# Kernel optimization log

Measured on AMD Instinct MI355X. Metric: run time of the kernel, lower is better.

The kernel has to match this reference:

```python
import jax, jax.numpy as jnp
import numpy as np

# FNO 2D spectral conv: rfft2 -> keep 2 corner mode blocks -> complex einsum -> scatter -> irfft2
B, H, W, CIN, COUT = 8, 256, 256, 32, 32
M1, M2 = 16, 16
SCALE = 1.0 / (CIN * COUT)  # matches self.scale = 1/(in_channels*out_channels)


def setup_inputs() -> dict:
    key = jax.random.key(0)
    k1, k2, k3 = jax.random.split(key, 3)
    x = jax.random.normal(k1, (B, H, W, CIN), dtype=jnp.float32)  # channels_last input
    wshape = (2, CIN, COUT, M1, M2)  # (2**(ndims-1), in_c, out_c, m1, m2)
    w_real = (jax.random.uniform(k2, wshape, dtype=jnp.float32) * 2.0 - 1.0) * SCALE
    w_imag = (jax.random.uniform(k3, wshape, dtype=jnp.float32) * 2.0 - 1.0) * SCALE
    return {"x": x, "w_real": w_real, "w_imag": w_imag}


def reference(x, w_real, w_imag):
    w = jax.lax.complex(w_real, w_imag)  # complex64 spectral weights
    # channels_last -> channels_first: [B,H,W,C] -> [B,C,H,W]
    xc = jnp.transpose(x, (0, 3, 1, 2))
    x_ft = jnp.fft.rfft2(xc)  # [B, C, H, W//2+1] complex64
    # Two corner blocks along dim H (low and high freqs), low freqs along rfft dim.
    blocks = jnp.stack(
        [x_ft[:, :, :M1, :M2], x_ft[:, :, H - M1:, :M2]], axis=0
    )  # [2, B, Cin, M1, M2]
    # einsum 'wbi...,wio...->w...bo' (reordered here to wbohk; scatter layout equivalent)
    ob = jnp.einsum('wbihk,wiohk->wbohk', blocks, w)  # [2, B, Cout, M1, M2]
    out_ft = jnp.zeros((B, COUT, H, W // 2 + 1), dtype=ob.dtype)
    out_ft = out_ft.at[:, :, :M1, :M2].set(ob[0])
    out_ft = out_ft.at[:, :, H - M1:, :M2].set(ob[1])
    out = jnp.fft.irfft2(out_ft, s=(H, W))  # [B, Cout, H, W] float32
    # back to channels_last; activation is None (identity)
    return jnp.transpose(out, (0, 2, 3, 1))
```

## Files before the change

kernel.cpp:

```cpp
#include <hip/hip_runtime.h>
#include <math.h>


#define INV_HW (1.0f / 65536.0f)

__global__ void k_tw(float* __restrict__ Eo, float* __restrict__ Ei,
                     float* __restrict__ U, float* __restrict__ E4) {
  int t = blockIdx.x * blockDim.x + threadIdx.x;
  const float step = 6.28318530717958647692f / 256.0f;
  if (t < 512) {
    int j = t & 3, kwq = (t >> 2) & 3, w1 = (t >> 4) & 15, ws = t >> 8;
    int kw = 4 * kwq + j, w = ws * 64 + 4 * w1;
    int m = (kw * w) & 255;
    float s, c; sincosf(step * (float)m, &s, &c);
    int base = ((ws * 16 + w1) * 4 + kwq) * 8 + 2 * j;
    Eo[base] = c; Eo[base + 1] = -s;
  } else if (t < 576) {
    int i = t - 512;
    int j = i & 3, w0 = (i >> 2) & 3, kwq = i >> 4;
    int kw = 4 * kwq + j;
    int m = (kw * w0) & 255;
    float s, c; sincosf(step * (float)m, &s, &c);
    int base = (kwq * 4 + w0) * 8 + 2 * j;
    Ei[base] = c; Ei[base + 1] = -s;
  } else if (t < 832) {
    int n = t - 576;
    float s, c; sincosf(step * (float)n, &s, &c);
    ((float2*)U)[n] = make_float2(c, s);
  } else if (t < 1856) {
    int i = t - 832;
    int w = i >> 3, q = i & 7;
    int me = (2 * q * w) & 255, mo = ((2 * q + 1) * w) & 255;
    float se, ce, so, co;
    sincosf(step * (float)me, &se, &ce);
    sincosf(step * (float)mo, &so, &co);
    float sc_e = (q == 0) ? INV_HW : 2.0f * INV_HW;
    float sc_o = 2.0f * INV_HW;
    ((float4*)E4)[i] = make_float4(sc_e * ce, sc_e * se, sc_o * co, sc_o * so);
  }
}

__global__ __launch_bounds__(256) void k_wdft(const float* __restrict__ x,
                                              const float* __restrict__ Eo,
                                              const float* __restrict__ Ei,
                                              float* __restrict__ T) {
  __shared__ __align__(16) float sx[8192];
  __shared__ __align__(16) float sEo[1024];
  __shared__ __align__(16) float sEi[128];
  int bh = blockIdx.x, t = threadIdx.x;
  const float4* src = (const float4*)(x + (size_t)bh * 8192);
  float4* dx = (float4*)sx;
#pragma unroll
  for (int i = 0; i < 8; ++i) dx[t + 256 * i] = src[t + 256 * i];
  ((float4*)sEo)[t] = ((const float4*)Eo)[t];
  if (t < 32) ((float4*)sEi)[t] = ((const float4*)Ei)[t];
  __syncthreads();
  int kwq = t >> 6, ws = (t >> 5) & 1, c = t & 31;
  float ar[4][4], ai[4][4];
#pragma unroll
  for (int a = 0; a < 4; ++a)
#pragma unroll
    for (int b = 0; b < 4; ++b) { ar[a][b] = 0.f; ai[a][b] = 0.f; }
  const float* xc = sx + c;
#pragma unroll 4
  for (int w1 = 0; w1 < 16; ++w1) {
    int wb = ws * 64 + 4 * w1;
    float xa0 = xc[(wb + 0) * 32], xa1 = xc[(wb + 1) * 32];
    float xa2 = xc[(wb + 2) * 32], xa3 = xc[(wb + 3) * 32];
    float xb0 = xc[(wb + 128) * 32], xb1 = xc[(wb + 129) * 32];
    float xb2 = xc[(wb + 130) * 32], xb3 = xc[(wb + 131) * 32];
    const float4* ep = (const float4*)(sEo + ((ws * 16 + w1) * 4 + kwq) * 8);
    float4 e01 = ep[0], e23 = ep[1];
    float ye, yo;
    ye = xa0 + xb0; yo = xa0 - xb0;
    ar[0][0] += ye * e01.x; ai[0][0] += ye * e01.y;
    ar[0][1] += yo * e01.z; ai[0][1] += yo * e01.w;
    ar[0][2] += ye * e23.x; ai[0][2] += ye * e23.y;
    ar[0][3] += yo * e23.z; ai[0][3] += yo * e23.w;
    ye = xa1 + xb1; yo = xa1 - xb1;
    ar[1][0] += ye * e01.x; ai[1][0] += ye * e01.y;
    ar[1][1] += yo * e01.z; ai[1][1] += yo * e01.w;
    ar[1][2] += ye * e23.x; ai[1][2] += ye * e23.y;
    ar[1][3] += yo * e23.z; ai[1][3] += yo * e23.w;
    ye = xa2 + xb2; yo = xa2 - xb2;
    ar[2][0] += ye * e01.x; ai[2][0] += ye * e01.y;
    ar[2][1] += yo * e01.z; ai[2][1] += yo * e01.w;
    ar[2][2] += ye * e23.x; ai[2][2] += ye * e23.y;
    ar[2][3] += yo * e23.z; ai[2][3] += yo * e23.w;
    ye = xa3 + xb3; yo = xa3 - xb3;
    ar[3][0] += ye * e01.x; ai[3][0] += ye * e01.y;
    ar[3][1] += yo * e01.z; ai[3][1] += yo * e01.w;
    ar[3][2] += ye * e23.x; ai[3][2] += ye * e23.y;
    ar[3][3] += yo * e23.z; ai[3][3] += yo * e23.w;
  }
  const float4* eip = (const float4*)(sEi + kwq * 32);
  float Tr[4] = {0, 0, 0, 0}, Ti[4] = {0, 0, 0, 0};
#pragma unroll
  for (int w0 = 0; w0 < 4; ++w0) {
    float4 g01 = eip[2 * w0], g23 = eip[2 * w0 + 1];
    Tr[0] += ar[w0][0] * g01.x - ai[w0][0] * g01.y;
    Ti[0] += ar[w0][0] * g01.y + ai[w0][0] * g01.x;
    Tr[1] += ar[w0][1] * g01.z - ai[w0][1] * g01.w;
    Ti[1] += ar[w0][1] * g01.w + ai[w0][1] * g01.z;
    Tr[2] += ar[w0][2] * g23.x - ai[w0][2] * g23.y;
    Ti[2] += ar[w0][2] * g23.y + ai[w0][2] * g23.x;
    Tr[3] += ar[w0][3] * g23.z - ai[w0][3] * g23.w;
    Ti[3] += ar[w0][3] * g23.w + ai[w0][3] * g23.z;
  }
#pragma unroll
  for (int j = 0; j < 4; ++j) {
    Tr[j] += __shfl_xor(Tr[j], 32);
    Ti[j] += __shfl_xor(Ti[j], 32);
  }
  if (ws == 0) {
    float* tp = T + (size_t)bh * 1024 + c * 32 + kwq * 8;
    *(float4*)tp = make_float4(Tr[0], Ti[0], Tr[1], Ti[1]);
    *(float4*)(tp + 4) = make_float4(Tr[2], Ti[2], Tr[3], Ti[3]);
  }
}

__global__ __launch_bounds__(256) void k_hdft(const float* __restrict__ T,
                                              const float* __restrict__ U,
                                              float* __restrict__ Xp) {
  __shared__ __align__(16) float sT[2048];
  __shared__ float2 sU[256];
  int bi = blockIdx.x;
  int b = bi >> 7, c = (bi >> 2) & 31, hq = bi & 3;
  int t = threadIdx.x;
#pragma unroll
  for (int it = 0; it < 2; ++it) {
    int idx = t + 256 * it;
    int row = idx >> 3, col = idx & 7;
    int h = hq * 32 + (row & 31) + (row >> 5) * 128;
    ((float4*)sT)[idx] =
        *(const float4*)(T + (size_t)(b * 256 + h) * 1024 + c * 32 + col * 4);
  }
  sU[t] = ((const float2*)U)[t];
  __syncthreads();
  int khp = t >> 4, kw = t & 15;
  int kha2 = khp + 240;
  float sg = (khp & 1) ? -1.f : 1.f;
  int f0 = hq * 32;
  int ph1 = (khp * f0) & 255, ph2 = (kha2 * f0) & 255;
  float x0r = 0, x0i = 0, x1r = 0, x1i = 0;
#pragma unroll 4
  for (int fl = 0; fl < 32; ++fl) {
    float2 t0 = *(const float2*)(sT + fl * 32 + kw * 2);
    float2 t1 = *(const float2*)(sT + (fl + 32) * 32 + kw * 2);
    float tpx = fmaf(sg, t1.x, t0.x);
    float tpy = fmaf(sg, t1.y, t0.y);
    float2 e1 = sU[ph1], e2 = sU[ph2];
    x0r += tpx * e1.x + tpy * e1.y;
    x0i += tpy * e1.x - tpx * e1.y;
    x1r += tpx * e2.x + tpy * e2.y;
    x1i += tpy * e2.x - tpx * e2.y;
    ph1 = (ph1 + khp) & 255;
    ph2 = (ph2 + kha2) & 255;
  }
  float2* xb = (float2*)(Xp + (size_t)(hq * 256 + b * 32 + c) * 1024);
  xb[khp * 16 + kw] = make_float2(x0r, x0i);
  xb[(khp + 16) * 16 + kw] = make_float2(x1r, x1i);
}

__global__ __launch_bounds__(256) void k_mix(const float* __restrict__ Xp,
                                             const float* __restrict__ wr,
                                             const float* __restrict__ wi_,
                                             float* __restrict__ Yp) {
  __shared__ __align__(16) float sX[1024];
  int bi = blockIdx.x;
  int b = bi >> 6, kh = (bi >> 1) & 31, ih = bi & 1;
  int blk = kh >> 4, khl = kh & 15;
  int t = threadIdx.x;
  {
    float4 acc = make_float4(0.f, 0.f, 0.f, 0.f);
#pragma unroll
    for (int hq = 0; hq < 4; ++hq) {
      float4 v = *(const float4*)(Xp + (size_t)(hq * 256 + b * 32 + (t >> 3)) * 1024 +
                                  kh * 32 + (t & 7) * 4);
      acc.x += v.x; acc.y += v.y; acc.z += v.z; acc.w += v.w;
    }
    ((float4*)sX)[t] = acc;
  }
  __syncthreads();
  int o = t >> 3, kwq = (t >> 1) & 3, is = t & 1;
  float yr[4] = {0, 0, 0, 0}, yi[4] = {0, 0, 0, 0};
  size_t wbase = (size_t)blk * 262144 + (size_t)o * 256 + khl * 16 + kwq * 4;
#pragma unroll
  for (int ii = 0; ii < 8; ++ii) {
    int i = ih * 16 + is * 8 + ii;
    float4 a = *(const float4*)(wr + wbase + (size_t)i * 8192);
    float4 bb = *(const float4*)(wi_ + wbase + (size_t)i * 8192);
    float4 x01 = *(const float4*)(sX + i * 32 + kwq * 8);
    float4 x23 = *(const float4*)(sX + i * 32 + kwq * 8 + 4);
    yr[0] += x01.x * a.x - x01.y * bb.x; yi[0] += x01.x * bb.x + x01.y * a.x;
    yr[1] += x01.z * a.y - x01.w * bb.y; yi[1] += x01.z * bb.y + x01.w * a.y;
    yr[2] += x23.x * a.z - x23.y * bb.z; yi[2] += x23.x * bb.z + x23.y * a.z;
    yr[3] += x23.z * a.w - x23.w * bb.w; yi[3] += x23.z * bb.w + x23.w * a.w;
  }
#pragma unroll
  for (int j = 0; j < 4; ++j) {
    yr[j] += __shfl_xor(yr[j], 1);
    yi[j] += __shfl_xor(yi[j], 1);
  }
  if (is == 0) {
    float* yp = Yp + (size_t)((ih * 8 + b) * 32 + o) * 1024 + kh * 32 + kwq * 8;
    *(float4*)yp = make_float4(yr[0], yi[0], yr[1], yi[1]);
    *(float4*)(yp + 4) = make_float4(yr[2], yi[2], yr[3], yi[3]);
  }
}

__global__ __launch_bounds__(256) void k_hidft(const float* __restrict__ Yp,
                                               const float* __restrict__ U,
                                               float* __restrict__ G) {
  __shared__ __align__(16) float4 sY4[256];
  __shared__ float2 sU[256];
  int bi = blockIdx.x;
  int b = bi >> 7, o = (bi >> 2) & 31, hc = bi & 3;
  int t = threadIdx.x;
  {
    float4 va = ((const float4*)(Yp + (size_t)(b * 32 + o) * 1024))[t];
    float4 vb = ((const float4*)(Yp + (size_t)(256 + b * 32 + o) * 1024))[t];
    sY4[t] = make_float4(va.x + vb.x, va.y + vb.y, va.z + vb.z, va.w + vb.w);
  }
  sU[t] = ((const float2*)U)[t];
  __syncthreads();
  int q = t & 7, hl = t >> 3;
  int h = hc * 32 + hl;
  float se0r = 0, se0i = 0, se1r = 0, se1i = 0;
  float so0r = 0, so0i = 0, so1r = 0, so1i = 0;
#pragma unroll 4
  for (int kh2 = 0; kh2 < 16; ++kh2) {
    int khe = 2 * kh2, kho = khe + 1;
    int khae = khe < 16 ? khe : khe + 224;
    int khao = kho < 16 ? kho : kho + 224;
    float2 ee = sU[(khae * h) & 255];
    float2 eo = sU[(khao * h) & 255];
    float4 yE = sY4[khe * 8 + q];
    float4 yO = sY4[kho * 8 + q];
    se0r += yE.x * ee.x - yE.y * ee.y;
    se0i += yE.x * ee.y + yE.y * ee.x;
    se1r += yE.z * ee.x - yE.w * ee.y;
    se1i += yE.z * ee.y + yE.w * ee.x;
    so0r += yO.x * eo.x - yO.y * eo.y;
    so0i += yO.x * eo.y + yO.y * eo.x;
    so1r += yO.z * eo.x - yO.w * eo.y;
    so1i += yO.z * eo.y + yO.w * eo.x;
  }
  float* g0 = G + (((size_t)b * 256 + h) * 32 + o) * 32 + 4 * q;
  float* g1 = G + (((size_t)b * 256 + h + 128) * 32 + o) * 32 + 4 * q;
  *(float4*)g0 = make_float4(se0r + so0r, se0i + so0i, se1r + so1r, se1i + so1i);
  *(float4*)g1 = make_float4(se0r - so0r, se0i - so0i, se1r - so1r, se1i - so1i);
}

__global__ __launch_bounds__(256) void k_widft(const float* __restrict__ G,
                                               const float* __restrict__ E4,
                                               float* __restrict__ out) {
  __shared__ __align__(16) float sG[1024];
  __shared__ __align__(16) float4 sE4[1024];
  int bh = blockIdx.x, t = threadIdx.x;
  ((float4*)sG)[t] = ((const float4*)(G + (size_t)bh * 1024))[t];
  const float4* e4g = (const float4*)E4;
#pragma unroll
  for (int i = 0; i < 4; ++i) sE4[t + 256 * i] = e4g[t + 256 * i];
  __syncthreads();
  int og = t >> 7, w = t & 127;
  float4 tw[8];
#pragma unroll
  for (int q = 0; q < 8; ++q) tw[q] = sE4[w * 8 + q];
  float* ob = out + (size_t)bh * 8192 + w * 32 + og * 16;
  float* ob2 = ob + 128 * 32;
#pragma unroll
  for (int g4 = 0; g4 < 4; ++g4) {
    float s0[4], s1[4];
#pragma unroll
    for (int k = 0; k < 4; ++k) {
      int o = og * 16 + g4 * 4 + k;
      const float4* gp = (const float4*)(sG + o * 32);
      float se = 0.f, so = 0.f;
#pragma unroll
      for (int q = 0; q < 8; ++q) {
        float4 g = gp[q];
        se += g.x * tw[q].x - g.y * tw[q].y;
        so += g.z * tw[q].z - g.w * tw[q].w;
      }
      s0[k] = se + so;
      s1[k] = se - so;
    }
    *(float4*)(ob + g4 * 4) = make_float4(s0[0], s0[1], s0[2], s0[3]);
    *(float4*)(ob2 + g4 * 4) = make_float4(s1[0], s1[1], s1[2], s1[3]);
  }
}

extern "C" void kernel_launch(void* const* d_in, const int* in_sizes, int n_in,
                              void* d_out, int out_size, void* d_ws, size_t ws_size,
                              hipStream_t stream) {
  const float* x = (const float*)d_in[0];
  const float* wr = (const float*)d_in[1];
  const float* wi = (const float*)d_in[2];
  float* out = (float*)d_out;
  float* ws = (float*)d_ws;

  float* Eo = ws;
  float* Ei = ws + 1024;
  float* U  = ws + 1280;
  float* E4 = ws + 1792;
  float* T  = ws + 6144;
  float* Xp = ws + 2103296;
  float* Yp = ws + 3151872;
  float* G  = T;

  k_tw<<<8, 256, 0, stream>>>(Eo, Ei, U, E4);
  k_wdft<<<2048, 256, 0, stream>>>(x, Eo, Ei, T);
  k_hdft<<<1024, 256, 0, stream>>>(T, U, Xp);
  k_mix<<<512, 256, 0, stream>>>(Xp, wr, wi, Yp);
  k_hidft<<<1024, 256, 0, stream>>>(Yp, U, G);
  k_widft<<<2048, 256, 0, stream>>>(G, E4, out);
}
```

Baseline: 169.6 us.

## Drop twiddle kernel, compute twiddles in-kernel, and read inputs directly from global

Removes the separate twiddle-precompute launch. Twiddle factors are now generated with sincosf inside k_wdft, k_hdft and k_hidft, and the E4 table is built by four extra blocks appended to the k_wdft grid. k_wdft and k_hdft no longer stage x and T in shared memory and instead read them straight from global. The k_wdft store is split across both ws halves so all threads write. This saves one launch and shared-memory staging, at the cost of redundant sincos work per block and strided, uncoalesced global loads.

```diff
diff --git a/kernel.cpp b/kernel.cpp
--- a/kernel.cpp
+++ b/kernel.cpp
@@ -3,57 +3,44 @@
 
 
 #define INV_HW (1.0f / 65536.0f)
-
-__global__ void k_tw(float* __restrict__ Eo, float* __restrict__ Ei,
-                     float* __restrict__ U, float* __restrict__ E4) {
-  int t = blockIdx.x * blockDim.x + threadIdx.x;
-  const float step = 6.28318530717958647692f / 256.0f;
-  if (t < 512) {
-    int j = t & 3, kwq = (t >> 2) & 3, w1 = (t >> 4) & 15, ws = t >> 8;
-    int kw = 4 * kwq + j, w = ws * 64 + 4 * w1;
-    int m = (kw * w) & 255;
-    float s, c; sincosf(step * (float)m, &s, &c);
-    int base = ((ws * 16 + w1) * 4 + kwq) * 8 + 2 * j;
-    Eo[base] = c; Eo[base + 1] = -s;
-  } else if (t < 576) {
-    int i = t - 512;
-    int j = i & 3, w0 = (i >> 2) & 3, kwq = i >> 4;
-    int kw = 4 * kwq + j;
-    int m = (kw * w0) & 255;
-    float s, c; sincosf(step * (float)m, &s, &c);
-    int base = (kwq * 4 + w0) * 8 + 2 * j;
-    Ei[base] = c; Ei[base + 1] = -s;
-  } else if (t < 832) {
-    int n = t - 576;
-    float s, c; sincosf(step * (float)n, &s, &c);
-    ((float2*)U)[n] = make_float2(c, s);
-  } else if (t < 1856) {
-    int i = t - 832;
+#define STEP 0.0245436926061702596f
+
+__global__ __launch_bounds__(256) void k_wdft(const float* __restrict__ x,
+                                              float* __restrict__ T,
+                                              float* __restrict__ E4) {
+  int bi = blockIdx.x, t = threadIdx.x;
+  if (bi >= 2048) {
+    int i = (bi - 2048) * 256 + t;
     int w = i >> 3, q = i & 7;
     int me = (2 * q * w) & 255, mo = ((2 * q + 1) * w) & 255;
     float se, ce, so, co;
-    sincosf(step * (float)me, &se, &ce);
-    sincosf(step * (float)mo, &so, &co);
+    sincosf(STEP * (float)me, &se, &ce);
+    sincosf(STEP * (float)mo, &so, &co);
     float sc_e = (q == 0) ? INV_HW : 2.0f * INV_HW;
     float sc_o = 2.0f * INV_HW;
     ((float4*)E4)[i] = make_float4(sc_e * ce, sc_e * se, sc_o * co, sc_o * so);
-  }
-}
-
-__global__ __launch_bounds__(256) void k_wdft(const float* __restrict__ x,
-                                              const float* __restrict__ Eo,
-                                              const float* __restrict__ Ei,
-                                              float* __restrict__ T) {
-  __shared__ __align__(16) float sx[8192];
+    return;
+  }
   __shared__ __align__(16) float sEo[1024];
   __shared__ __align__(16) float sEi[128];
-  int bh = blockIdx.x, t = threadIdx.x;
-  const float4* src = (const float4*)(x + (size_t)bh * 8192);
-  float4* dx = (float4*)sx;
-#pragma unroll
-  for (int i = 0; i < 8; ++i) dx[t + 256 * i] = src[t + 256 * i];
-  ((float4*)sEo)[t] = ((const float4*)Eo)[t];
-  if (t < 32) ((float4*)sEi)[t] = ((const float4*)Ei)[t];
+  {
+    int half = t & 1, kwq = (t >> 1) & 3, u = t >> 3;
+    int kw0 = 4 * kwq + 2 * half, kw1 = kw0 + 1;
+    int m0 = (kw0 * 4 * u) & 255, m1 = (kw1 * 4 * u) & 255;
+    float s0, c0, s1, c1;
+    sincosf(STEP * (float)m0, &s0, &c0);
+    sincosf(STEP * (float)m1, &s1, &c1);
+    ((float4*)sEo)[t] = make_float4(c0, -s0, c1, -s1);
+    if (t < 32) {
+      int h2 = t & 1, w0 = (t >> 1) & 3, kq = t >> 3;
+      int ka = 4 * kq + 2 * h2, kb = ka + 1;
+      int ma = (ka * w0) & 255, mb = (kb * w0) & 255;
+      float sa, ca, sb, cb;
+      sincosf(STEP * (float)ma, &sa, &ca);
+      sincosf(STEP * (float)mb, &sb, &cb);
+      ((float4*)sEi)[t] = make_float4(ca, -sa, cb, -sb);
+    }
+  }
   __syncthreads();
   int kwq = t >> 6, ws = (t >> 5) & 1, c = t & 31;
   float ar[4][4], ai[4][4];
@@ -61,7 +48,7 @@
   for (int a = 0; a < 4; ++a)
 #pragma unroll
     for (int b = 0; b < 4; ++b) { ar[a][b] = 0.f; ai[a][b] = 0.f; }
-  const float* xc = sx + c;
+  const float* xc = x + (size_t)bi * 8192 + c;
 #pragma unroll 4
   for (int w1 = 0; w1 < 16; ++w1) {
     int wb = ws * 64 + 4 * w1;
@@ -112,32 +99,25 @@
     Tr[j] += __shfl_xor(Tr[j], 32);
     Ti[j] += __shfl_xor(Ti[j], 32);
   }
-  if (ws == 0) {
-    float* tp = T + (size_t)bh * 1024 + c * 32 + kwq * 8;
-    *(float4*)tp = make_float4(Tr[0], Ti[0], Tr[1], Ti[1]);
-    *(float4*)(tp + 4) = make_float4(Tr[2], Ti[2], Tr[3], Ti[3]);
-  }
+  float4 v = ws ? make_float4(Tr[2], Ti[2], Tr[3], Ti[3])
+               : make_float4(Tr[0], Ti[0], Tr[1], Ti[1]);
+  *(float4*)(T + (size_t)bi * 1024 + c * 32 + kwq * 8 + ws * 4) = v;
 }
 
 __global__ __launch_bounds__(256) void k_hdft(const float* __restrict__ T,
-                                              const float* __restrict__ U,
                                               float* __restrict__ Xp) {
-  __shared__ __align__(16) float sT[2048];
   __shared__ float2 sU[256];
   int bi = blockIdx.x;
   int b = bi >> 7, c = (bi >> 2) & 31, hq = bi & 3;
   int t = threadIdx.x;
-#pragma unroll
-  for (int it = 0; it < 2; ++it) {
-    int idx = t + 256 * it;
-    int row = idx >> 3, col = idx & 7;
-    int h = hq * 32 + (row & 31) + (row >> 5) * 128;
-    ((float4*)sT)[idx] =
-        *(const float4*)(T + (size_t)(b * 256 + h) * 1024 + c * 32 + col * 4);
-  }
-  sU[t] = ((const float2*)U)[t];
+  {
+    float s, cc;
+    sincosf(STEP * (float)t, &s, &cc);
+    sU[t] = make_float2(cc, s);
+  }
   __syncthreads();
   int khp = t >> 4, kw = t & 15;
+  const float* Tb = T + (size_t)b * 262144 + c * 32 + kw * 2;
   int kha2 = khp + 240;
   float sg = (khp & 1) ? -1.f : 1.f;
   int f0 = hq * 32;
@@ -145,8 +125,9 @@
   float x0r = 0, x0i = 0, x1r = 0, x1i = 0;
 #pragma unroll 4
   for (int fl = 0; fl < 32; ++fl) {
-    float2 t0 = *(const float2*)(sT + fl * 32 + kw * 2);
-    float2 t1 = *(const float2*)(sT + (fl + 32) * 32 + kw * 2);
+    int h = hq * 32 + fl;
+    float2 t0 = *(const float2*)(Tb + (size_t)h * 1024);
+    float2 t1 = *(const float2*)(Tb + (size_t)(h + 128) * 1024);
     float tpx = fmaf(sg, t1.x, t0.x);
     float tpy = fmaf(sg, t1.y, t0.y);
     float2 e1 = sU[ph1], e2 = sU[ph2];
@@ -210,7 +191,6 @@
 }
 
 __global__ __launch_bounds__(256) void k_hidft(const float* __restrict__ Yp,
-                                               const float* __restrict__ U,
                                                float* __restrict__ G) {
   __shared__ __align__(16) float4 sY4[256];
   __shared__ float2 sU[256];
@@ -221,8 +201,10 @@
     float4 va = ((const float4*)(Yp + (size_t)(b * 32 + o) * 1024))[t];
     float4 vb = ((const float4*)(Yp + (size_t)(256 + b * 32 + o) * 1024))[t];
     sY4[t] = make_float4(va.x + vb.x, va.y + vb.y, va.z + vb.z, va.w + vb.w);
-  }
-  sU[t] = ((const float2*)U)[t];
+    float s, cc;
+    sincosf(STEP * (float)t, &s, &cc);
+    sU[t] = make_float2(cc, s);
+  }
   __syncthreads();
   int q = t & 7, hl = t >> 3;
   int h = hc * 32 + hl;
@@ -300,19 +282,15 @@
   float* out = (float*)d_out;
   float* ws = (float*)d_ws;
 
-  float* Eo = ws;
-  float* Ei = ws + 1024;
-  float* U  = ws + 1280;
-  float* E4 = ws + 1792;
-  float* T  = ws + 6144;
-  float* Xp = ws + 2103296;
-  float* Yp = ws + 3151872;
+  float* E4 = ws;
+  float* T  = ws + 4096;
+  float* Xp = ws + 2101248;
+  float* Yp = ws + 3149824;
   float* G  = T;
 
-  k_tw<<<8, 256, 0, stream>>>(Eo, Ei, U, E4);
-  k_wdft<<<2048, 256, 0, stream>>>(x, Eo, Ei, T);
-  k_hdft<<<1024, 256, 0, stream>>>(T, U, Xp);
+  k_wdft<<<2052, 256, 0, stream>>>(x, T, E4);
+  k_hdft<<<1024, 256, 0, stream>>>(T, Xp);
   k_mix<<<512, 256, 0, stream>>>(Xp, wr, wi, Yp);
-  k_hidft<<<1024, 256, 0, stream>>>(Yp, U, G);
+  k_hidft<<<1024, 256, 0, stream>>>(Yp, G);
   k_widft<<<2048, 256, 0, stream>>>(G, E4, out);
 }
```

Result: slower. 175.6 us (+3.5%).
